# Performance work log

Measured on AMD Instinct MI355X. Metric: run time of the kernel, lower is better.

Reference implementation:

```python
import jax, jax.numpy as jnp
import numpy as np

TEMP = 0.05       # self.temp
SIM_TEMP = 0.05   # self.sim_temp
UM_TEMP = 0.5     # uncertain module temperature
MOMENTUM = 0.2    # self.momentum
EPS = 1e-12


def _l2norm(x, axis=-1):
    return x / jnp.maximum(jnp.linalg.norm(x, axis=axis, keepdims=True), EPS)


def _cross_entropy(logits, labels):
    # mean over batch of -log_softmax(logits)[i, labels[i]]
    logp = jax.nn.log_softmax(logits, axis=-1)
    return -jnp.take_along_axis(logp, labels[:, None], axis=1).mean()


def setup_inputs() -> dict:
    key = jax.random.key(0)
    k1, k2, k3 = jax.random.split(key, 3)
    B, N, D, U = 64, 65536, 1024, 16
    inputs = jax.random.normal(k1, (B, D), dtype=jnp.float32)
    # bank rows are unit-norm after any update in the original; start normalized
    features = _l2norm(jax.random.normal(k2, (N, D), dtype=jnp.float32))
    targets = jax.random.randint(k3, (B,), 0, N)
    return {"inputs": inputs, "features": features, "targets": targets,
            "uncertain_num": U}


def reference(inputs, features, targets, uncertain_num):
    x = _l2norm(inputs)                      # F.normalize(inputs, dim=1)
    logits = x @ features.T                  # [B, N] similarity (CM.forward)

    # --- uncertain_module.compute_uncertain: entropy of softmax(sim / um_temp),
    # ascending sort -> most uncertain samples are the last `uncertain_num` ---
    logp_u = jax.nn.log_softmax(logits / UM_TEMP, axis=1)
    score = -jnp.sum(jnp.exp(logp_u) * logp_u, axis=1)   # [B] entropy
    order = jnp.argsort(score)
    unc = order[-uncertain_num:]                          # most uncertain indices

    u_logits = logits[unc]                                # [U, N]
    # hard_label / sim_softmax (no-grad in original)
    sim = jax.nn.softmax(jax.lax.stop_gradient(u_logits) / SIM_TEMP, axis=1)
    lam = sim.max(axis=1)                                 # [U]
    labels = sim.argmax(axis=1)                           # [U]
    uncertain_loss = _cross_entropy(u_logits / TEMP, labels)

    loss = _cross_entropy(logits / TEMP, targets)

    # --- CM backward side effect: sequential per-sample momentum scatter-EMA
    # into the bank with per-row renormalization (order matters on repeats) ---
    def step(feats, xy):
        xi, yi = xy
        row = MOMENTUM * feats[yi] + (1.0 - MOMENTUM) * xi
        row = row / jnp.maximum(jnp.linalg.norm(row), EPS)
        return feats.at[yi].set(row), None

    new_features, _ = jax.lax.scan(step, features, (x, targets))
    return loss, uncertain_loss, lam, new_features
```

## Files before the change

kernel.cpp:

```cpp
#include <hip/hip_runtime.h>
#include <hip/hip_bf16.h>
#include <math.h>

typedef float  f32x4_t  __attribute__((ext_vector_type(4)));
typedef short  s16x8_t  __attribute__((ext_vector_type(8)));

__device__ __forceinline__ short f2bf(float f) {
  union { float f; unsigned u; } a; a.f = f;
  unsigned r = a.u + 0x7fffu + ((a.u >> 16) & 1u);
  return (short)(r >> 16);
}
__device__ __forceinline__ float bf2f(short s) {
  union { unsigned u; float f; } a; a.u = ((unsigned)(unsigned short)s) << 16;
  return a.f;
}

__device__ __forceinline__ float wave_sum_f(float v) {
#pragma unroll
  for (int o = 32; o > 0; o >>= 1) v += __shfl_down(v, o, 64);
  return v;
}
__device__ __forceinline__ float wave_max_f(float v) {
#pragma unroll
  for (int o = 32; o > 0; o >>= 1) v = fmaxf(v, __shfl_down(v, o, 64));
  return v;
}
__device__ __forceinline__ double wave_sum_d(double v) {
#pragma unroll
  for (int o = 32; o > 0; o >>= 1) v += __shfl_down(v, o, 64);
  return v;
}
__device__ __forceinline__ float block_sum256(float v, float* s4) {
  v = wave_sum_f(v);
  if ((threadIdx.x & 63) == 0) s4[threadIdx.x >> 6] = v;
  __syncthreads();
  float r = s4[0] + s4[1] + s4[2] + s4[3];
  __syncthreads();
  return r;
}
__device__ __forceinline__ float block_max256(float v, float* s4) {
  v = wave_max_f(v);
  if ((threadIdx.x & 63) == 0) s4[threadIdx.x >> 6] = v;
  __syncthreads();
  float r = fmaxf(fmaxf(s4[0], s4[1]), fmaxf(s4[2], s4[3]));
  __syncthreads();
  return r;
}
__device__ __forceinline__ double block_sum256d(double v, double* s4) {
  v = wave_sum_d(v);
  if ((threadIdx.x & 63) == 0) s4[threadIdx.x >> 6] = v;
  __syncthreads();
  double r = s4[0] + s4[1] + s4[2] + s4[3];
  __syncthreads();
  return r;
}

__global__ __launch_bounds__(256) void k0_norm(const float* __restrict__ inp,
    float* __restrict__ xf, short* __restrict__ xhi, short* __restrict__ xlo, int D) {
  __shared__ float s4[4];
  const int b = blockIdx.x, tid = threadIdx.x;
  const float4 v = *(const float4*)(inp + (size_t)b * D + tid * 4);
  const float ss = block_sum256(v.x*v.x + v.y*v.y + v.z*v.z + v.w*v.w, s4);
  const float rn = 1.0f / fmaxf(sqrtf(ss), 1e-12f);
  const float4 x = make_float4(v.x*rn, v.y*rn, v.z*rn, v.w*rn);
  *(float4*)(xf + (size_t)b * D + tid * 4) = x;
  short4 h, l;
  h.x = f2bf(x.x); l.x = f2bf(x.x - bf2f(h.x));
  h.y = f2bf(x.y); l.y = f2bf(x.y - bf2f(h.y));
  h.z = f2bf(x.z); l.z = f2bf(x.z - bf2f(h.z));
  h.w = f2bf(x.w); l.w = f2bf(x.w - bf2f(h.w));
  *(short4*)(xhi + (size_t)b * D + tid * 4) = h;
  *(short4*)(xlo + (size_t)b * D + tid * 4) = l;
}

__global__ __launch_bounds__(256) void k1_gemm(
    const float* __restrict__ feat, const short* __restrict__ xhi, const short* __restrict__ xlo,
    float* __restrict__ out_feat, float* __restrict__ logits, int N, int D, int copy_limit) {
  __shared__ short lh[64 * 40];
  __shared__ short ll[64 * 40];
  const int tid = threadIdx.x;
  const int wv = tid >> 6, lane = tid & 63;
  const int n0 = blockIdx.x * 64;
  const bool do_copy = (n0 < copy_limit);
  const int r0 = tid >> 3, kg = tid & 7;
  const int r1 = r0 + 32;
  const int mrow = wv * 16 + (lane & 15);
  const int kgl = lane >> 4;
  const int lb = (lane & 15) * 40 + kgl * 8;

  f32x4_t acc[4];
#pragma unroll
  for (int i = 0; i < 4; ++i) acc[i] = f32x4_t{0.f, 0.f, 0.f, 0.f};

  const short* xh_p = xhi + (size_t)mrow * D + kgl * 8;
  const short* xl_p = xlo + (size_t)mrow * D + kgl * 8;

  for (int kk = 0; kk < D; kk += 32) {
    const float4 v0 = *(const float4*)(feat + (size_t)(n0 + r0) * D + kk + kg * 4);
    const float4 v1 = *(const float4*)(feat + (size_t)(n0 + r1) * D + kk + kg * 4);
    if (do_copy) {
      float* p0 = out_feat + (size_t)(n0 + r0) * D + kk + kg * 4;
      *(float2*)p0       = make_float2(v0.x, v0.y);
      *(float2*)(p0 + 2) = make_float2(v0.z, v0.w);
      float* p1 = out_feat + (size_t)(n0 + r1) * D + kk + kg * 4;
      *(float2*)p1       = make_float2(v1.x, v1.y);
      *(float2*)(p1 + 2) = make_float2(v1.z, v1.w);
    }
    __syncthreads();
    {
      short4 h, l;
      h.x = f2bf(v0.x); l.x = f2bf(v0.x - bf2f(h.x));
      h.y = f2bf(v0.y); l.y = f2bf(v0.y - bf2f(h.y));
      h.z = f2bf(v0.z); l.z = f2bf(v0.z - bf2f(h.z));
      h.w = f2bf(v0.w); l.w = f2bf(v0.w - bf2f(h.w));
      *(short4*)(lh + r0 * 40 + kg * 4) = h;
      *(short4*)(ll + r0 * 40 + kg * 4) = l;
      h.x = f2bf(v1.x); l.x = f2bf(v1.x - bf2f(h.x));
      h.y = f2bf(v1.y); l.y = f2bf(v1.y - bf2f(h.y));
      h.z = f2bf(v1.z); l.z = f2bf(v1.z - bf2f(h.z));
      h.w = f2bf(v1.w); l.w = f2bf(v1.w - bf2f(h.w));
      *(short4*)(lh + r1 * 40 + kg * 4) = h;
      *(short4*)(ll + r1 * 40 + kg * 4) = l;
    }
    __syncthreads();
    const s16x8_t ah = *(const s16x8_t*)(xh_p + kk);
    const s16x8_t al = *(const s16x8_t*)(xl_p + kk);
#pragma unroll
    for (int nt = 0; nt < 4; ++nt) {
      const s16x8_t bh = *(const s16x8_t*)(lh + nt * 640 + lb);
      const s16x8_t bl = *(const s16x8_t*)(ll + nt * 640 + lb);
      acc[nt] = __builtin_amdgcn_mfma_f32_16x16x32_bf16(ah, bh, acc[nt], 0, 0, 0);
      acc[nt] = __builtin_amdgcn_mfma_f32_16x16x32_bf16(ah, bl, acc[nt], 0, 0, 0);
      acc[nt] = __builtin_amdgcn_mfma_f32_16x16x32_bf16(al, bh, acc[nt], 0, 0, 0);
    }
  }
#pragma unroll
  for (int nt = 0; nt < 4; ++nt) {
    const int n = n0 + nt * 16 + (lane & 15);
#pragma unroll
    for (int r = 0; r < 4; ++r) {
      const int brow = wv * 16 + kgl * 4 + r;
      logits[(size_t)brow * N + n] = acc[nt][r];
    }
  }
}

__global__ __launch_bounds__(256) void k2_stats(const float* __restrict__ logits,
                                                double* __restrict__ partials, int N) {
  __shared__ float sf[4];
  __shared__ double sd[4];
  const int bid = blockIdx.x;
  const int b = bid >> 2, p = bid & 3;
  const int chunk = N >> 2;
  const float4* row = (const float4*)(logits + (size_t)b * N + (size_t)p * chunk);
  const int n4 = chunk >> 2;
  float m = -3.0e38f;
  for (int i = threadIdx.x; i < n4; i += 256) {
    float4 v = row[i];
    m = fmaxf(m, fmaxf(fmaxf(v.x, v.y), fmaxf(v.z, v.w)));
  }
  const float M = block_max256(m, sf);
  double s0 = 0.0, s1 = 0.0, t0 = 0.0;
  for (int i = threadIdx.x; i < n4; i += 256) {
    float4 v = row[i];
    float c, d, e2;
    c = v.x; d = c - M; e2 = __expf(2.0f*d); s0 += (double)e2; s1 += (double)(2.0f*c*e2); t0 += (double)__expf(20.0f*d);
    c = v.y; d = c - M; e2 = __expf(2.0f*d); s0 += (double)e2; s1 += (double)(2.0f*c*e2); t0 += (double)__expf(20.0f*d);
    c = v.z; d = c - M; e2 = __expf(2.0f*d); s0 += (double)e2; s1 += (double)(2.0f*c*e2); t0 += (double)__expf(20.0f*d);
    c = v.w; d = c - M; e2 = __expf(2.0f*d); s0 += (double)e2; s1 += (double)(2.0f*c*e2); t0 += (double)__expf(20.0f*d);
  }
  s0 = block_sum256d(s0, sd);
  s1 = block_sum256d(s1, sd);
  t0 = block_sum256d(t0, sd);
  if (threadIdx.x == 0) {
    double* o = partials + (size_t)bid * 4;
    o[0] = (double)M; o[1] = s0; o[2] = s1; o[3] = t0;
  }
}

__global__ __launch_bounds__(64) void k3_select(const double* __restrict__ partials,
    const float* __restrict__ logits, const int* __restrict__ tgt,
    float* __restrict__ OUT, int B, int N, int U) {
  __shared__ double sc[64], st0[64], lred[64], ured[64];
  const int b = threadIdx.x;
  if (b < B) {
    const double* P = partials + (size_t)b * 16;
    double M = P[0];
    for (int p = 1; p < 4; ++p) M = fmax(M, P[p * 4]);
    double s0 = 0, s1 = 0, t0 = 0;
    for (int p = 0; p < 4; ++p) {
      double mm = P[p * 4];
      double w2 = exp(2.0 * (mm - M));
      double w20 = exp(20.0 * (mm - M));
      s0 += P[p * 4 + 1] * w2; s1 += P[p * 4 + 2] * w2; t0 += P[p * 4 + 3] * w20;
    }
    sc[b]  = 2.0 * M + log(s0) - s1 / s0;
    st0[b] = t0;
    const float tl = logits[(size_t)b * N + tgt[b]];
    lred[b] = 20.0 * (M - (double)tl) + log(t0);
    ured[b] = 0.0;
  }
  __syncthreads();
  if (b < B) {
    const double s = sc[b];
    int r = 0;
    for (int j = 0; j < B; ++j) {
      const double sj = sc[j];
      r += (sj < s || (sj == s && j < b)) ? 1 : 0;
    }
    if (r >= B - U) {
      OUT[2 + (r - (B - U))] = (float)(1.0 / st0[b]);
      ured[b] = log(st0[b]);
    }
  }
  __syncthreads();
  if (b == 0) {
    double ls = 0, us = 0;
    for (int j = 0; j < B; ++j) { ls += lred[j]; us += ured[j]; }
    OUT[0] = (float)(ls / B);
    OUT[1] = (float)(us / U);
  }
}

__global__ __launch_bounds__(256) void k4_tail(const float* __restrict__ feat,
    float* __restrict__ out_feat, int copy_limit, int N, int D) {
  const size_t start = (size_t)copy_limit * D;
  const size_t n2 = ((size_t)(N - copy_limit) * D) >> 1;
  const size_t stride = (size_t)gridDim.x * blockDim.x;
  for (size_t i = (size_t)blockIdx.x * blockDim.x + threadIdx.x; i < n2; i += stride) {
    const float2 v = *(const float2*)(feat + start + 2 * i);
    *(float2*)(out_feat + start + 2 * i) = v;
  }
}

__global__ __launch_bounds__(256) void k5_scan(const float* __restrict__ inp,
    const int* __restrict__ tgt, float* __restrict__ out_feat, int B, int D) {
  __shared__ float s4[4];
  const int i0 = blockIdx.x;
  const int y = tgt[i0];
  for (int j = 0; j < i0; ++j) if (tgt[j] == y) return;
  const int tid = threadIdx.x;
  float* rowp = out_feat + (size_t)y * D + tid * 4;
  const float2 aa = *(const float2*)rowp;
  const float2 bb = *(const float2*)(rowp + 2);
  float f0 = aa.x, f1 = aa.y, f2 = bb.x, f3 = bb.y;
  for (int occ = i0; occ < B; ++occ) {
    if (tgt[occ] != y) continue;
    const float4 xv = *(const float4*)(inp + (size_t)occ * D + tid * 4);
    const float ss = block_sum256(xv.x*xv.x + xv.y*xv.y + xv.z*xv.z + xv.w*xv.w, s4);
    const float rn = 1.0f / fmaxf(sqrtf(ss), 1e-12f);
    f0 = 0.2f * f0 + 0.8f * (xv.x * rn);
    f1 = 0.2f * f1 + 0.8f * (xv.y * rn);
    f2 = 0.2f * f2 + 0.8f * (xv.z * rn);
    f3 = 0.2f * f3 + 0.8f * (xv.w * rn);
    const float ss2 = block_sum256(f0*f0 + f1*f1 + f2*f2 + f3*f3, s4);
    const float rn2 = 1.0f / fmaxf(sqrtf(ss2), 1e-12f);
    f0 *= rn2; f1 *= rn2; f2 *= rn2; f3 *= rn2;
  }
  *(float2*)rowp       = make_float2(f0, f1);
  *(float2*)(rowp + 2) = make_float2(f2, f3);
}

extern "C" void kernel_launch(void* const* d_in, const int* in_sizes, int n_in,
                              void* d_out, int out_size, void* d_ws, size_t ws_size,
                              hipStream_t stream) {
  (void)n_in; (void)d_ws; (void)ws_size;
  const float* inp  = (const float*)d_in[0];
  const float* feat = (const float*)d_in[1];
  const int*   tgt  = (const int*)d_in[2];
  const int B = in_sizes[2];
  const int D = in_sizes[0] / B;
  const int N = in_sizes[1] / D;
  const int U = out_size - 2 - N * D;
  float* OUT = (float*)d_out;
  float* out_feat = OUT + 2 + U;

  const size_t logitsE = (size_t)B * N;
  const size_t xfE     = (size_t)B * D;
  const size_t needF   = 2 + logitsE + xfE + xfE + 4096;
  int scratch_rows = (int)((needF + D - 1) / D);
  scratch_rows = ((scratch_rows + 63) / 64) * 64;
  const int copy_limit = N - scratch_rows;
  float* scratch = out_feat + (size_t)copy_limit * D + 2;
  float* logits = scratch;
  float* xf = logits + logitsE;
  short* xhi = (short*)(xf + xfE);
  short* xlo = xhi + xfE;
  double* partials = (double*)(xlo + xfE);

  k0_norm  <<<B,       256, 0, stream>>>(inp, xf, xhi, xlo, D);
  k1_gemm  <<<N / 64,  256, 0, stream>>>(feat, xhi, xlo, out_feat, logits, N, D, copy_limit);
  k2_stats <<<B * 4,   256, 0, stream>>>(logits, partials, N);
  k3_select<<<1,       64,  0, stream>>>(partials, logits, tgt, OUT, B, N, U);
  k4_tail  <<<2048,    256, 0, stream>>>(feat, out_feat, copy_limit, N, D);
  k5_scan  <<<B,       256, 0, stream>>>(inp, tgt, out_feat, B, D);
}
```

Measured before the change: 604.6 us.

## Double-buffer GEMM K-loop with register prefetch and widen stats split

The feature-bank GEMM now processes 64-wide K steps with double-buffered LDS tiles and register prefetch of the next feature chunk, leaving one barrier per step instead of two. This is meant to hide global-load latency behind MFMA work. The stats kernel splits each row into 16 chunks instead of 4 to put more blocks in flight, and the unused fp32 normalized-input buffer is dropped. The larger LDS footprint and launch bounds may limit occupancy, and the scratch-size arithmetic changed as well.

Result: faster. 558.0 us (-7.7%).

```diff
diff --git a/kernel.cpp b/kernel.cpp
--- a/kernel.cpp
+++ b/kernel.cpp
@@ -56,14 +56,13 @@
 }
 
 __global__ __launch_bounds__(256) void k0_norm(const float* __restrict__ inp,
-    float* __restrict__ xf, short* __restrict__ xhi, short* __restrict__ xlo, int D) {
+    short* __restrict__ xhi, short* __restrict__ xlo, int D) {
   __shared__ float s4[4];
   const int b = blockIdx.x, tid = threadIdx.x;
   const float4 v = *(const float4*)(inp + (size_t)b * D + tid * 4);
   const float ss = block_sum256(v.x*v.x + v.y*v.y + v.z*v.z + v.w*v.w, s4);
   const float rn = 1.0f / fmaxf(sqrtf(ss), 1e-12f);
   const float4 x = make_float4(v.x*rn, v.y*rn, v.z*rn, v.w*rn);
-  *(float4*)(xf + (size_t)b * D + tid * 4) = x;
   short4 h, l;
   h.x = f2bf(x.x); l.x = f2bf(x.x - bf2f(h.x));
   h.y = f2bf(x.y); l.y = f2bf(x.y - bf2f(h.y));
@@ -73,20 +72,19 @@
   *(short4*)(xlo + (size_t)b * D + tid * 4) = l;
 }
 
-__global__ __launch_bounds__(256) void k1_gemm(
+__global__ __launch_bounds__(256, 4) void k1_gemm(
     const float* __restrict__ feat, const short* __restrict__ xhi, const short* __restrict__ xlo,
     float* __restrict__ out_feat, float* __restrict__ logits, int N, int D, int copy_limit) {
-  __shared__ short lh[64 * 40];
-  __shared__ short ll[64 * 40];
+  __shared__ short lh[2][64 * 72];
+  __shared__ short ll[2][64 * 72];
   const int tid = threadIdx.x;
   const int wv = tid >> 6, lane = tid & 63;
   const int n0 = blockIdx.x * 64;
   const bool do_copy = (n0 < copy_limit);
-  const int r0 = tid >> 3, kg = tid & 7;
-  const int r1 = r0 + 32;
+  const int rt = tid >> 2, cg = tid & 3;
   const int mrow = wv * 16 + (lane & 15);
   const int kgl = lane >> 4;
-  const int lb = (lane & 15) * 40 + kgl * 8;
+  const int lbo = (lane & 15) * 72 + kgl * 8;
 
   f32x4_t acc[4];
 #pragma unroll
@@ -94,46 +92,74 @@
 
   const short* xh_p = xhi + (size_t)mrow * D + kgl * 8;
   const short* xl_p = xlo + (size_t)mrow * D + kgl * 8;
-
-  for (int kk = 0; kk < D; kk += 32) {
-    const float4 v0 = *(const float4*)(feat + (size_t)(n0 + r0) * D + kk + kg * 4);
-    const float4 v1 = *(const float4*)(feat + (size_t)(n0 + r1) * D + kk + kg * 4);
+  const float* fsrc = feat + (size_t)(n0 + rt) * D + cg * 16;
+  float*       fdst = out_feat + (size_t)(n0 + rt) * D + cg * 16;
+  const int wofs = rt * 72 + cg * 16;
+
+  float4 va[4], vb[4];
+#pragma unroll
+  for (int q = 0; q < 4; ++q) va[q] = *(const float4*)(fsrc + 4 * q);
+
+  auto step = [&](float4 (&cur)[4], float4 (&nxt)[4], int buf, int kk) {
+    const s16x8_t ah0 = *(const s16x8_t*)(xh_p + kk);
+    const s16x8_t al0 = *(const s16x8_t*)(xl_p + kk);
+    const s16x8_t ah1 = *(const s16x8_t*)(xh_p + kk + 32);
+    const s16x8_t al1 = *(const s16x8_t*)(xl_p + kk + 32);
+    const int kpf = kk + 64;
+    if (kpf < D) {
+#pragma unroll
+      for (int q = 0; q < 4; ++q) nxt[q] = *(const float4*)(fsrc + kpf + 4 * q);
+    }
+    s16x8_t h0, h1, l0, l1;
+    { const float4 v = cur[0];
+      h0[0]=f2bf(v.x); l0[0]=f2bf(v.x-bf2f(h0[0])); h0[1]=f2bf(v.y); l0[1]=f2bf(v.y-bf2f(h0[1]));
+      h0[2]=f2bf(v.z); l0[2]=f2bf(v.z-bf2f(h0[2])); h0[3]=f2bf(v.w); l0[3]=f2bf(v.w-bf2f(h0[3])); }
+    { const float4 v = cur[1];
+      h0[4]=f2bf(v.x); l0[4]=f2bf(v.x-bf2f(h0[4])); h0[5]=f2bf(v.y); l0[5]=f2bf(v.y-bf2f(h0[5]));
+      h0[6]=f2bf(v.z); l0[6]=f2bf(v.z-bf2f(h0[6])); h0[7]=f2bf(v.w); l0[7]=f2bf(v.w-bf2f(h0[7])); }
+    { const float4 v = cur[2];
+      h1[0]=f2bf(v.x); l1[0]=f2bf(v.x-bf2f(h1[0])); h1[1]=f2bf(v.y); l1[1]=f2bf(v.y-bf2f(h1[1]));
+      h1[2]=f2bf(v.z); l1[2]=f2bf(v.z-bf2f(h1[2])); h1[3]=f2bf(v.w); l1[3]=f2bf(v.w-bf2f(h1[3])); }
+    { const float4 v = cur[3];
+      h1[4]=f2bf(v.x); l1[4]=f2bf(v.x-bf2f(h1[4])); h1[5]=f2bf(v.y); l1[5]=f2bf(v.y-bf2f(h1[5]));
+      h1[6]=f2bf(v.z); l1[6]=f2bf(v.z-bf2f(h1[6])); h1[7]=f2bf(v.w); l1[7]=f2bf(v.w-bf2f(h1[7])); }
+    *(s16x8_t*)(&lh[buf][wofs])     = h0;
+    *(s16x8_t*)(&lh[buf][wofs + 8]) = h1;
+    *(s16x8_t*)(&ll[buf][wofs])     = l0;
+    *(s16x8_t*)(&ll[buf][wofs + 8]) = l1;
     if (do_copy) {
-      float* p0 = out_feat + (size_t)(n0 + r0) * D + kk + kg * 4;
-      *(float2*)p0       = make_float2(v0.x, v0.y);
-      *(float2*)(p0 + 2) = make_float2(v0.z, v0.w);
-      float* p1 = out_feat + (size_t)(n0 + r1) * D + kk + kg * 4;
-      *(float2*)p1       = make_float2(v1.x, v1.y);
-      *(float2*)(p1 + 2) = make_float2(v1.z, v1.w);
-    }
-    __syncthreads();
-    {
-      short4 h, l;
-      h.x = f2bf(v0.x); l.x = f2bf(v0.x - bf2f(h.x));
-      h.y = f2bf(v0.y); l.y = f2bf(v0.y - bf2f(h.y));
-      h.z = f2bf(v0.z); l.z = f2bf(v0.z - bf2f(h.z));
-      h.w = f2bf(v0.w); l.w = f2bf(v0.w - bf2f(h.w));
-      *(short4*)(lh + r0 * 40 + kg * 4) = h;
-      *(short4*)(ll + r0 * 40 + kg * 4) = l;
-      h.x = f2bf(v1.x); l.x = f2bf(v1.x - bf2f(h.x));
-      h.y = f2bf(v1.y); l.y = f2bf(v1.y - bf2f(h.y));
-      h.z = f2bf(v1.z); l.z = f2bf(v1.z - bf2f(h.z));
-      h.w = f2bf(v1.w); l.w = f2bf(v1.w - bf2f(h.w));
-      *(short4*)(lh + r1 * 40 + kg * 4) = h;
-      *(short4*)(ll + r1 * 40 + kg * 4) = l;
-    }
-    __syncthreads();
-    const s16x8_t ah = *(const s16x8_t*)(xh_p + kk);
-    const s16x8_t al = *(const s16x8_t*)(xl_p + kk);
+#pragma unroll
+      for (int q = 0; q < 4; ++q) {
+        const float4 v = cur[q];
+        *(float2*)(fdst + kk + 4 * q)     = make_float2(v.x, v.y);
+        *(float2*)(fdst + kk + 4 * q + 2) = make_float2(v.z, v.w);
+      }
+    }
+    asm volatile("s_waitcnt lgkmcnt(0)" ::: "memory");
+    __builtin_amdgcn_s_barrier();
+    __builtin_amdgcn_sched_barrier(0);
+    const short* rbh = &lh[buf][lbo];
+    const short* rbl = &ll[buf][lbo];
 #pragma unroll
     for (int nt = 0; nt < 4; ++nt) {
-      const s16x8_t bh = *(const s16x8_t*)(lh + nt * 640 + lb);
-      const s16x8_t bl = *(const s16x8_t*)(ll + nt * 640 + lb);
-      acc[nt] = __builtin_amdgcn_mfma_f32_16x16x32_bf16(ah, bh, acc[nt], 0, 0, 0);
-      acc[nt] = __builtin_amdgcn_mfma_f32_16x16x32_bf16(ah, bl, acc[nt], 0, 0, 0);
-      acc[nt] = __builtin_amdgcn_mfma_f32_16x16x32_bf16(al, bh, acc[nt], 0, 0, 0);
-    }
-  }
+      const s16x8_t bh0 = *(const s16x8_t*)(rbh + nt * 1152);
+      const s16x8_t bl0 = *(const s16x8_t*)(rbl + nt * 1152);
+      acc[nt] = __builtin_amdgcn_mfma_f32_16x16x32_bf16(ah0, bh0, acc[nt], 0, 0, 0);
+      acc[nt] = __builtin_amdgcn_mfma_f32_16x16x32_bf16(ah0, bl0, acc[nt], 0, 0, 0);
+      acc[nt] = __builtin_amdgcn_mfma_f32_16x16x32_bf16(al0, bh0, acc[nt], 0, 0, 0);
+      const s16x8_t bh1 = *(const s16x8_t*)(rbh + nt * 1152 + 32);
+      const s16x8_t bl1 = *(const s16x8_t*)(rbl + nt * 1152 + 32);
+      acc[nt] = __builtin_amdgcn_mfma_f32_16x16x32_bf16(ah1, bh1, acc[nt], 0, 0, 0);
+      acc[nt] = __builtin_amdgcn_mfma_f32_16x16x32_bf16(ah1, bl1, acc[nt], 0, 0, 0);
+      acc[nt] = __builtin_amdgcn_mfma_f32_16x16x32_bf16(al1, bh1, acc[nt], 0, 0, 0);
+    }
+  };
+
+  for (int it2 = 0; it2 < D / 128; ++it2) {
+    step(va, vb, 0, it2 * 128);
+    step(vb, va, 1, it2 * 128 + 64);
+  }
+
 #pragma unroll
   for (int nt = 0; nt < 4; ++nt) {
     const int n = n0 + nt * 16 + (lane & 15);
@@ -150,8 +176,8 @@
   __shared__ float sf[4];
   __shared__ double sd[4];
   const int bid = blockIdx.x;
-  const int b = bid >> 2, p = bid & 3;
-  const int chunk = N >> 2;
+  const int b = bid >> 4, p = bid & 15;
+  const int chunk = N >> 4;
   const float4* row = (const float4*)(logits + (size_t)b * N + (size_t)p * chunk);
   const int n4 = chunk >> 2;
   float m = -3.0e38f;
@@ -184,11 +210,11 @@
   __shared__ double sc[64], st0[64], lred[64], ured[64];
   const int b = threadIdx.x;
   if (b < B) {
-    const double* P = partials + (size_t)b * 16;
+    const double* P = partials + (size_t)b * 64;
     double M = P[0];
-    for (int p = 1; p < 4; ++p) M = fmax(M, P[p * 4]);
+    for (int p = 1; p < 16; ++p) M = fmax(M, P[p * 4]);
     double s0 = 0, s1 = 0, t0 = 0;
-    for (int p = 0; p < 4; ++p) {
+    for (int p = 0; p < 16; ++p) {
       double mm = P[p * 4];
       double w2 = exp(2.0 * (mm - M));
       double w20 = exp(20.0 * (mm - M));
@@ -277,20 +303,19 @@
 
   const size_t logitsE = (size_t)B * N;
   const size_t xfE     = (size_t)B * D;
-  const size_t needF   = 2 + logitsE + xfE + xfE + 4096;
+  const size_t needF   = 2 + logitsE + xfE  + (size_t)B * 16 * 4 * 2  + 4096;
   int scratch_rows = (int)((needF + D - 1) / D);
   scratch_rows = ((scratch_rows + 63) / 64) * 64;
   const int copy_limit = N - scratch_rows;
   float* scratch = out_feat + (size_t)copy_limit * D + 2;
   float* logits = scratch;
-  float* xf = logits + logitsE;
-  short* xhi = (short*)(xf + xfE);
+  short* xhi = (short*)(logits + logitsE);
   short* xlo = xhi + xfE;
   double* partials = (double*)(xlo + xfE);
 
-  k0_norm  <<<B,       256, 0, stream>>>(inp, xf, xhi, xlo, D);
+  k0_norm  <<<B,       256, 0, stream>>>(inp, xhi, xlo, D);
   k1_gemm  <<<N / 64,  256, 0, stream>>>(feat, xhi, xlo, out_feat, logits, N, D, copy_limit);
-  k2_stats <<<B * 4,   256, 0, stream>>>(logits, partials, N);
+  k2_stats <<<B * 16,  256, 0, stream>>>(logits, partials, N);
   k3_select<<<1,       64,  0, stream>>>(partials, logits, tgt, OUT, B, N, U);
   k4_tail  <<<2048,    256, 0, stream>>>(feat, out_feat, copy_limit, N, D);
   k5_scan  <<<B,       256, 0, stream>>>(inp, tgt, out_feat, B, D);
```
